# Performance work log

Measured on AMD Instinct MI355X. Metric: run time of the kernel, lower is better.

The kernel has to match this reference:

```python
import jax, jax.numpy as jnp
import numpy as np

EPS_LN = 1e-5
NEG_SLOPE = 0.2
NUM_GRAPHS = 64


def layer_norm(h, g, b):
    mu = h.mean(-1, keepdims=True)
    var = ((h - mu) ** 2).mean(-1, keepdims=True)
    return (h - mu) * jax.lax.rsqrt(var + EPS_LN) * g + b


def segment_softmax(alpha, dst, n):
    # alpha: [E2, H], softmax over edges sharing the same dst node
    m = jax.ops.segment_max(alpha, dst, num_segments=n)
    m = jnp.where(jnp.isfinite(m), m, 0.0)
    e = jnp.exp(alpha - m[dst])
    s = jax.ops.segment_sum(e, dst, num_segments=n)
    return e / (s[dst] + 1e-16)


def gat_conv(h, src, dst, eattr, W, We, a_s, a_d, a_e, bias, H, C):
    # PyG GATConv: shared src/dst linear, edge features, self-loops (fill='mean')
    N = h.shape[0]
    x = (h @ W).reshape(N, H, C)  # [N,H,C]
    loop = jnp.arange(N)
    src2 = jnp.concatenate([src, loop])
    dst2 = jnp.concatenate([dst, loop])
    loop_attr = jnp.broadcast_to(eattr.mean(0, keepdims=True), (N, eattr.shape[1]))
    e2 = jnp.concatenate([eattr, loop_attr], 0)
    eh = (e2 @ We).reshape(-1, H, C)  # [E2,H,C]
    alpha = (x * a_s).sum(-1)[src2] + (x * a_d).sum(-1)[dst2] + (eh * a_e).sum(-1)
    alpha = jax.nn.leaky_relu(alpha, NEG_SLOPE)  # [E2,H]
    alpha = segment_softmax(alpha, dst2, N)
    out = jax.ops.segment_sum(x[src2] * alpha[:, :, None], dst2, num_segments=N)
    return out.reshape(N, H * C) + bias


def setup_inputs():
    key = jax.random.key(0)
    ks = jax.random.split(key, 24)
    N, E = 50000, 400000
    Fin, Hd, H, ed = 6, 64, 4, 1
    d0 = Hd * H          # 256 after layer0
    C1 = 128 // H        # 32, layer1 per-head out
    s = 0.1
    inp = {
        'x': jax.random.normal(ks[0], (N, Fin), jnp.float32),
        'edge_index': jax.random.randint(ks[1], (2, E), 0, N),
        'edge_attr': jax.random.uniform(ks[2], (E, ed), jnp.float32),
        'batch': jnp.sort(jax.random.randint(ks[3], (N,), 0, NUM_GRAPHS)),
        'W_in': jax.random.normal(ks[4], (Fin, Hd), jnp.float32) * s,
        'b_in': jnp.zeros((Hd,), jnp.float32),
        'l0_W': jax.random.normal(ks[5], (Hd, H * Hd), jnp.float32) * s,
        'l0_We': jax.random.normal(ks[6], (ed, H * Hd), jnp.float32) * s,
        'l0_as': jax.random.normal(ks[7], (H, Hd), jnp.float32) * s,
        'l0_ad': jax.random.normal(ks[8], (H, Hd), jnp.float32) * s,
        'l0_ae': jax.random.normal(ks[9], (H, Hd), jnp.float32) * s,
        'l0_b': jnp.zeros((H * Hd,), jnp.float32),
        'ln0_g': jnp.ones((d0,), jnp.float32),
        'ln0_b': jnp.zeros((d0,), jnp.float32),
        'l1_W': jax.random.normal(ks[10], (d0, H * C1), jnp.float32) * s,
        'l1_We': jax.random.normal(ks[11], (ed, H * C1), jnp.float32) * s,
        'l1_as': jax.random.normal(ks[12], (H, C1), jnp.float32) * s,
        'l1_ad': jax.random.normal(ks[13], (H, C1), jnp.float32) * s,
        'l1_ae': jax.random.normal(ks[14], (H, C1), jnp.float32) * s,
        'l1_b': jnp.zeros((H * C1,), jnp.float32),
        'ln1_g': jnp.ones((128,), jnp.float32),
        'ln1_b': jnp.zeros((128,), jnp.float32),
    }
    return inp


def reference(x, edge_index, edge_attr, batch, W_in, b_in,
              l0_W, l0_We, l0_as, l0_ad, l0_ae, l0_b, ln0_g, ln0_b,
              l1_W, l1_We, l1_as, l1_ad, l1_ae, l1_b, ln1_g, ln1_b):
    src, dst = edge_index[0], edge_index[1]
    H = 4
    h = x @ W_in + b_in                                  # input_proj
    h = gat_conv(h, src, dst, edge_attr, l0_W, l0_We, l0_as, l0_ad, l0_ae, l0_b, H, 64)
    h = layer_norm(h, ln0_g, ln0_b)
    h = jax.nn.elu(h)                                    # dropout off (eval)
    h = gat_conv(h, src, dst, edge_attr, l1_W, l1_We, l1_as, l1_ad, l1_ae, l1_b, H, 32)
    h = layer_norm(h, ln1_g, ln1_b)
    cnt = jax.ops.segment_sum(jnp.ones((h.shape[0],), h.dtype), batch, num_segments=NUM_GRAPHS)
    h_mean = jax.ops.segment_sum(h, batch, num_segments=NUM_GRAPHS) / jnp.maximum(cnt, 1.0)[:, None]
    h_max = jax.ops.segment_max(h, batch, num_segments=NUM_GRAPHS)
    return (h_mean + h_max) / 2.0
```

## Files before the change

### kernel.cpp

```cpp
#include <hip/hip_runtime.h>
#include <math.h>

#define EPS_LN   1e-5f
#define NEG_SLOPE 0.2f
#define NUM_GRAPHS 64
#define POOL_SPLIT 16

__device__ __forceinline__ float red64(float v) {
    #pragma unroll
    for (int m = 32; m > 0; m >>= 1) v += __shfl_xor(v, m);
    return v;
}
__device__ __forceinline__ float red32(float v) {
    #pragma unroll
    for (int m = 16; m > 0; m >>= 1) v += __shfl_xor(v, m);
    return v;
}

__global__ __launch_bounds__(256) void k_input_proj(
    const float* __restrict__ x, const float* __restrict__ Win,
    const float* __restrict__ bin, float* __restrict__ h, int N)
{
    int t = blockIdx.x * 256 + threadIdx.x;
    if (t >= N * 64) return;
    int n = t >> 6, c = t & 63;
    float acc = bin[c];
    const float* xr = x + n * 6;
    #pragma unroll
    for (int k = 0; k < 6; ++k) acc += xr[k] * Win[k * 64 + c];
    h[t] = acc;
}

__global__ __launch_bounds__(256) void k_prep(
    const float* __restrict__ We0, const float* __restrict__ ae0,
    const float* __restrict__ We1, const float* __restrict__ ae1,
    float* __restrict__ wedot0, float* __restrict__ wedot1)
{
    __shared__ float red[256];
    int t = threadIdx.x;
    red[t] = We0[t] * ae0[t];
    __syncthreads();
    for (int s = 32; s > 0; s >>= 1) { if ((t & 63) < s) red[t] += red[t + s]; __syncthreads(); }
    if ((t & 63) == 0) wedot0[t >> 6] = red[t];
    __syncthreads();
    red[t] = (t < 128) ? We1[t] * ae1[t] : 0.f;
    __syncthreads();
    for (int s = 16; s > 0; s >>= 1) { if (t < 128 && (t & 31) < s) red[t] += red[t + s]; __syncthreads(); }
    if (t < 128 && (t & 31) == 0) wedot1[t >> 5] = red[t];
}

__global__ __launch_bounds__(256) void k_esum_partial(const float* __restrict__ ea, float* __restrict__ part, int E)
{
    __shared__ float red[256];
    int t = threadIdx.x;
    float s = 0.f;
    for (int i = blockIdx.x * 256 + t; i < E; i += gridDim.x * 256) s += ea[i];
    red[t] = s; __syncthreads();
    for (int k = 128; k > 0; k >>= 1) { if (t < k) red[t] += red[t + k]; __syncthreads(); }
    if (t == 0) part[blockIdx.x] = red[0];
}
__global__ __launch_bounds__(256) void k_esum_final(const float* __restrict__ part, int B, float* __restrict__ mean_out, int E)
{
    __shared__ float red[256];
    int t = threadIdx.x;
    red[t] = (t < B) ? part[t] : 0.f; __syncthreads();
    for (int k = 128; k > 0; k >>= 1) { if (t < k) red[t] += red[t + k]; __syncthreads(); }
    if (t == 0) *mean_out = red[0] / (float)E;
}

__global__ __launch_bounds__(256) void k_counts_init(int* __restrict__ counts, int N)
{
    int t = blockIdx.x * 256 + threadIdx.x;
    if (t < N) counts[t] = 1;
}
__global__ __launch_bounds__(256) void k_count(const int* __restrict__ dst, int* __restrict__ counts, int E)
{
    int e = blockIdx.x * 256 + threadIdx.x;
    if (e < E) atomicAdd(&counts[dst[e]], 1);
}
__global__ __launch_bounds__(256) void k_scan_partial(const int* __restrict__ counts, int* __restrict__ bsum, int N)
{
    __shared__ int red[256];
    int b = blockIdx.x, t = threadIdx.x;
    int base = b * 1024 + t * 4;
    int s = 0;
    #pragma unroll
    for (int i = 0; i < 4; ++i) { int idx = base + i; if (idx < N) s += counts[idx]; }
    red[t] = s; __syncthreads();
    for (int k = 128; k > 0; k >>= 1) { if (t < k) red[t] += red[t + k]; __syncthreads(); }
    if (t == 0) bsum[b] = red[0];
}
__global__ __launch_bounds__(64) void k_scan_bsums(const int* __restrict__ bsum, int* __restrict__ bpre, int B)
{
    __shared__ int s[64];
    int t = threadIdx.x;
    int v = (t < B) ? bsum[t] : 0;
    s[t] = v; __syncthreads();
    for (int off = 1; off < 64; off <<= 1) {
        int u = (t >= off) ? s[t - off] : 0; __syncthreads();
        s[t] += u; __syncthreads();
    }
    if (t < B) bpre[t] = s[t] - v;
}
__global__ __launch_bounds__(256) void k_scan_chunk(
    const int* __restrict__ counts, const int* __restrict__ bpre,
    int* __restrict__ row_ptr, int N, int E2)
{
    __shared__ int s[256];
    int b = blockIdx.x, t = threadIdx.x;
    int base = b * 1024 + t * 4;
    int l0 = (base + 0 < N) ? counts[base + 0] : 0;
    int l1 = (base + 1 < N) ? counts[base + 1] : 0;
    int l2 = (base + 2 < N) ? counts[base + 2] : 0;
    int l3 = (base + 3 < N) ? counts[base + 3] : 0;
    int lsum = l0 + l1 + l2 + l3;
    s[t] = lsum; __syncthreads();
    for (int off = 1; off < 256; off <<= 1) {
        int u = (t >= off) ? s[t - off] : 0; __syncthreads();
        s[t] += u; __syncthreads();
    }
    int run = bpre[b] + s[t] - lsum;
    if (base + 0 < N) row_ptr[base + 0] = run; run += l0;
    if (base + 1 < N) row_ptr[base + 1] = run; run += l1;
    if (base + 2 < N) row_ptr[base + 2] = run; run += l2;
    if (base + 3 < N) row_ptr[base + 3] = run;
    if (b == 0 && t == 0) row_ptr[N] = E2;
}
__global__ __launch_bounds__(256) void k_cursor_init(const int* __restrict__ row_ptr, int* __restrict__ cursor, int N)
{
    int t = blockIdx.x * 256 + threadIdx.x;
    if (t < N) cursor[t] = row_ptr[t];
}
__global__ __launch_bounds__(256) void k_place(
    const int* __restrict__ dst, int* __restrict__ cursor, int* __restrict__ eids, int E, int N)
{
    int e = blockIdx.x * 256 + threadIdx.x;
    if (e >= E + N) return;
    int d = (e < E) ? dst[e] : (e - E);
    int pos = atomicAdd(&cursor[d], 1);
    eids[pos] = e;
}
__global__ __launch_bounds__(256) void k_rowsort(const int* __restrict__ row_ptr, int* __restrict__ eids, int N)
{
    int n = blockIdx.x * 256 + threadIdx.x;
    if (n >= N) return;
    int r0 = row_ptr[n], r1 = row_ptr[n + 1];
    for (int i = r0 + 1; i < r1; ++i) {
        int key = eids[i];
        int j = i - 1;
        while (j >= r0 && eids[j] > key) { eids[j + 1] = eids[j]; --j; }
        eids[j + 1] = key;
    }
}

#define G0_NPW 4
__global__ __launch_bounds__(256) void k_gemm0(
    const float* __restrict__ h, const float* __restrict__ W0, float* __restrict__ x0, int N)
{
    __shared__ float Wl[64 * 256];
    int t = threadIdx.x;
    for (int i = t; i < 64 * 256; i += 256) Wl[i] = W0[i];
    __syncthreads();
    int wave = t >> 6, lane = t & 63;
    int gw = blockIdx.x * 4 + wave;
    int stride = gridDim.x * 4 * G0_NPW;
    for (int nb = gw * G0_NPW; nb < N; nb += stride) {
        float hv[G0_NPW];
        float acc[G0_NPW][4] = {};
        #pragma unroll
        for (int p = 0; p < G0_NPW; ++p) {
            int n = nb + p;
            hv[p] = (n < N) ? h[(size_t)n * 64 + lane] : 0.f;
        }
        for (int k = 0; k < 64; ++k) {
            float w0 = Wl[k * 256 + lane];
            float w1 = Wl[k * 256 + lane + 64];
            float w2 = Wl[k * 256 + lane + 128];
            float w3 = Wl[k * 256 + lane + 192];
            #pragma unroll
            for (int p = 0; p < G0_NPW; ++p) {
                float hk = __shfl(hv[p], k);
                acc[p][0] += hk * w0; acc[p][1] += hk * w1;
                acc[p][2] += hk * w2; acc[p][3] += hk * w3;
            }
        }
        #pragma unroll
        for (int p = 0; p < G0_NPW; ++p) {
            int n = nb + p;
            if (n < N) {
                float* o = x0 + (size_t)n * 256;
                o[lane] = acc[p][0]; o[lane + 64] = acc[p][1];
                o[lane + 128] = acc[p][2]; o[lane + 192] = acc[p][3];
            }
        }
    }
}

__global__ __launch_bounds__(256) void k_gemm1(
    const float* __restrict__ h0, const float* __restrict__ W1,
    float* __restrict__ x1, int N)
{
    __shared__ float Wc[32 * 128];
    __shared__ float Ht[32 * 128];
    const int nb = blockIdx.x * 128;
    const int t = threadIdx.x;
    const int tc = t & 15, tr = t >> 4;
    const int r0 = tr * 4, c0 = tc * 4;
    const int kg = t & 7, rb = t >> 3;
    float acc[8][8] = {};
    for (int kc = 0; kc < 8; ++kc) {
        __syncthreads();
        #pragma unroll
        for (int j = 0; j < 4; ++j) {
            int row = rb + j * 32;
            int n = nb + row;
            float4 v = make_float4(0.f, 0.f, 0.f, 0.f);
            if (n < N)
                v = *reinterpret_cast<const float4*>(h0 + (size_t)n * 256 + kc * 32 + kg * 4);
            #pragma unroll
            for (int i = 0; i < 4; ++i) {
                int k = kg * 4 + i;
                float e = (i == 0) ? v.x : (i == 1) ? v.y : (i == 2) ? v.z : v.w;
                Ht[k * 128 + (row ^ (k & 28))] = e;
            }
        }
        #pragma unroll
        for (int it = 0; it < 4; ++it) {
            int idx = t * 4 + it * 1024;
            int k2 = idx >> 7, c = idx & 127;
            *reinterpret_cast<float4*>(&Wc[idx]) =
                *reinterpret_cast<const float4*>(W1 + (size_t)(kc * 32 + k2) * 128 + c);
        }
        __syncthreads();
        #pragma unroll 4
        for (int k2 = 0; k2 < 32; ++k2) {
            int sw = k2 & 28;
            float4 hlo = *reinterpret_cast<const float4*>(&Ht[k2 * 128 + (r0 ^ sw)]);
            float4 hhi = *reinterpret_cast<const float4*>(&Ht[k2 * 128 + ((r0 + 64) ^ sw)]);
            float4 wlo = *reinterpret_cast<const float4*>(&Wc[k2 * 128 + c0]);
            float4 whi = *reinterpret_cast<const float4*>(&Wc[k2 * 128 + c0 + 64]);
            float hr[8] = {hlo.x, hlo.y, hlo.z, hlo.w, hhi.x, hhi.y, hhi.z, hhi.w};
            float wr[8] = {wlo.x, wlo.y, wlo.z, wlo.w, whi.x, whi.y, whi.z, whi.w};
            #pragma unroll
            for (int i = 0; i < 8; ++i)
                #pragma unroll
                for (int j = 0; j < 8; ++j)
                    acc[i][j] += hr[i] * wr[j];
        }
    }
    #pragma unroll
    for (int i = 0; i < 8; ++i) {
        int n = nb + ((i < 4) ? (r0 + i) : (r0 + 60 + i));
        if (n < N) {
            *reinterpret_cast<float4*>(x1 + (size_t)n * 128 + c0) =
                make_float4(acc[i][0], acc[i][1], acc[i][2], acc[i][3]);
            *reinterpret_cast<float4*>(x1 + (size_t)n * 128 + c0 + 64) =
                make_float4(acc[i][4], acc[i][5], acc[i][6], acc[i][7]);
        }
    }
}

template <int HC>
__global__ __launch_bounds__(256) void k_attn(
    const float* __restrict__ x, const float* __restrict__ a_s, const float* __restrict__ a_d,
    float* __restrict__ as_n, float* __restrict__ ad_n, int N)
{
    int n = (blockIdx.x * 256 + threadIdx.x) >> 6;
    int lane = threadIdx.x & 63;
    if (n >= N) return;
    const float* xr = x + (size_t)n * HC;
    #pragma unroll
    for (int j = 0; j < HC / 64; ++j) {
        int ch = j * 64 + lane;
        float v = xr[ch];
        float ps = v * a_s[ch], pd = v * a_d[ch];
        if (HC == 256) {
            ps = red64(ps); pd = red64(pd);
            if (lane == 0) { as_n[n * 4 + j] = ps; ad_n[n * 4 + j] = pd; }
        } else {
            ps = red32(ps); pd = red32(pd);
            if ((lane & 31) == 0) {
                int hh = 2 * j + (lane >> 5);
                as_n[n * 4 + hh] = ps; ad_n[n * 4 + hh] = pd;
            }
        }
    }
}

template <bool WRITE_SRC>
__global__ __launch_bounds__(256) void k_edgeprep(
    const int* __restrict__ row_ptr, const int* __restrict__ eids,
    const int* __restrict__ src, const float* __restrict__ eattr,
    const float* __restrict__ emean_p, const float* __restrict__ wedot,
    const float* __restrict__ as_n, const float* __restrict__ ad_n,
    int* __restrict__ srcp, float4* __restrict__ alpha, int N, int E)
{
    int n = (blockIdx.x * 256 + threadIdx.x) >> 6;
    int lane = threadIdx.x & 63;
    if (n >= N) return;
    float emean = *emean_p;
    float wd0 = wedot[0], wd1 = wedot[1], wd2 = wedot[2], wd3 = wedot[3];
    float adv0 = ad_n[n * 4 + 0], adv1 = ad_n[n * 4 + 1];
    float adv2 = ad_n[n * 4 + 2], adv3 = ad_n[n * 4 + 3];
    int r0 = row_ptr[n], r1 = row_ptr[n + 1];
    for (int i = r0 + lane; i < r1; i += 64) {
        int eid = eids[i];
        int sn; float ev;
        if (eid < E) { sn = src[eid]; ev = eattr[eid]; } else { sn = n; ev = emean; }
        if (WRITE_SRC) srcp[i] = sn;
        const float* as4 = as_n + (size_t)sn * 4;
        float a0 = as4[0] + adv0 + ev * wd0;
        float a1 = as4[1] + adv1 + ev * wd1;
        float a2 = as4[2] + adv2 + ev * wd2;
        float a3 = as4[3] + adv3 + ev * wd3;
        a0 = (a0 > 0.f) ? a0 : NEG_SLOPE * a0;
        a1 = (a1 > 0.f) ? a1 : NEG_SLOPE * a1;
        a2 = (a2 > 0.f) ? a2 : NEG_SLOPE * a2;
        a3 = (a3 > 0.f) ? a3 : NEG_SLOPE * a3;
        alpha[i] = make_float4(a0, a1, a2, a3);
    }
}

template <int HC, int VEC, bool DO_ELU>
__global__ __launch_bounds__(256) void k_agg(
    const float* __restrict__ x, const int* __restrict__ row_ptr,
    const int* __restrict__ srcp, const float* __restrict__ alpha,
    const float* __restrict__ bias, const float* __restrict__ lng, const float* __restrict__ lnb,
    float* __restrict__ out, int N)
{
    int n = (blockIdx.x * 256 + threadIdx.x) >> 6;
    int lane = threadIdx.x & 63;
    if (n >= N) return;
    int hh = lane >> 4;
    int r0 = row_ptr[n], r1 = row_ptr[n + 1];

    float m = -INFINITY, s = 0.f;
    float acc[VEC] = {};
    for (int i = r0; i < r1; ++i) {
        int sn = srcp[i];
        float a = alpha[(size_t)i * 4 + hh];
        float nm = fmaxf(m, a);
        float sc = __expf(m - nm);
        float w  = __expf(a - nm);
        m = nm;
        s = s * sc + w;
        const float* xr = x + (size_t)sn * HC + lane * VEC;
        if constexpr (VEC == 4) {
            float4 xv = *reinterpret_cast<const float4*>(xr);
            acc[0] = acc[0] * sc + w * xv.x;
            acc[1] = acc[1] * sc + w * xv.y;
            acc[2] = acc[2] * sc + w * xv.z;
            acc[3] = acc[3] * sc + w * xv.w;
        } else {
            float2 xv = *reinterpret_cast<const float2*>(xr);
            acc[0] = acc[0] * sc + w * xv.x;
            acc[1] = acc[1] * sc + w * xv.y;
        }
    }
    float inv = 1.f / (s + 1e-16f);

    int ch0 = lane * VEC;
    float v[VEC];
    #pragma unroll
    for (int i = 0; i < VEC; ++i) v[i] = acc[i] * inv + bias[ch0 + i];
    float ls = 0.f;
    #pragma unroll
    for (int i = 0; i < VEC; ++i) ls += v[i];
    ls = red64(ls);
    float mu = ls / (float)HC;
    float lv = 0.f;
    #pragma unroll
    for (int i = 0; i < VEC; ++i) { float d = v[i] - mu; lv += d * d; }
    lv = red64(lv);
    float rs = rsqrtf(lv / (float)HC + EPS_LN);
    float o[VEC];
    #pragma unroll
    for (int i = 0; i < VEC; ++i) {
        float y = (v[i] - mu) * rs * lng[ch0 + i] + lnb[ch0 + i];
        if (DO_ELU) y = (y > 0.f) ? y : (expm1f(y));
        o[i] = y;
    }
    float* orow = out + (size_t)n * HC + ch0;
    if constexpr (VEC == 4) *reinterpret_cast<float4*>(orow) = make_float4(o[0], o[1], o[2], o[3]);
    else                    *reinterpret_cast<float2*>(orow) = make_float2(o[0], o[1]);
}

__global__ __launch_bounds__(128) void k_bounds(const int* __restrict__ batch, int* __restrict__ gstart, int N)
{
    int g = threadIdx.x;
    if (g > NUM_GRAPHS) return;
    int lo = 0, hi = N;
    while (lo < hi) { int mid = (lo + hi) >> 1; if (batch[mid] < g) lo = mid + 1; else hi = mid; }
    gstart[g] = lo;
}
__global__ __launch_bounds__(128) void k_pool1(
    const float* __restrict__ h1, const int* __restrict__ gstart,
    float* __restrict__ psum, float* __restrict__ pmax)
{
    int g = blockIdx.x, sl = blockIdx.y, c = threadIdx.x;
    int s0 = gstart[g], s1 = gstart[g + 1];
    int cnt = s1 - s0;
    int chunk = (cnt + POOL_SPLIT - 1) / POOL_SPLIT;
    int b0 = s0 + sl * chunk;
    int b1 = min(b0 + chunk, s1);
    float sum = 0.f, mx = -INFINITY;
    for (int n = b0; n < b1; ++n) {
        float v = h1[(size_t)n * 128 + c];
        sum += v; mx = fmaxf(mx, v);
    }
    int o = (g * POOL_SPLIT + sl) * 128 + c;
    psum[o] = sum; pmax[o] = mx;
}
__global__ __launch_bounds__(128) void k_pool2(
    const float* __restrict__ psum, const float* __restrict__ pmax,
    const int* __restrict__ gstart, float* __restrict__ out)
{
    int g = blockIdx.x, c = threadIdx.x;
    float sum = 0.f, mx = -INFINITY;
    #pragma unroll
    for (int sl = 0; sl < POOL_SPLIT; ++sl) {
        int o = (g * POOL_SPLIT + sl) * 128 + c;
        sum += psum[o];
        mx = fmaxf(mx, pmax[o]);
    }
    int cnt = gstart[g + 1] - gstart[g];
    float mean = sum / fmaxf((float)cnt, 1.f);
    out[g * 128 + c] = 0.5f * (mean + mx);
}

extern "C" void kernel_launch(void* const* d_in, const int* in_sizes, int n_in,
                              void* d_out, int out_size, void* d_ws, size_t ws_size,
                              hipStream_t stream)
{
    const float* x     = (const float*)d_in[0];
    const int*   ei    = (const int*)d_in[1];
    const float* eattr = (const float*)d_in[2];
    const int*   batch = (const int*)d_in[3];
    const float* Win   = (const float*)d_in[4];
    const float* bin   = (const float*)d_in[5];
    const float* l0W   = (const float*)d_in[6];
    const float* l0We  = (const float*)d_in[7];
    const float* l0as  = (const float*)d_in[8];
    const float* l0ad  = (const float*)d_in[9];
    const float* l0ae  = (const float*)d_in[10];
    const float* l0b   = (const float*)d_in[11];
    const float* ln0g  = (const float*)d_in[12];
    const float* ln0b  = (const float*)d_in[13];
    const float* l1W   = (const float*)d_in[14];
    const float* l1We  = (const float*)d_in[15];
    const float* l1as  = (const float*)d_in[16];
    const float* l1ad  = (const float*)d_in[17];
    const float* l1ae  = (const float*)d_in[18];
    const float* l1b   = (const float*)d_in[19];
    const float* ln1g  = (const float*)d_in[20];
    const float* ln1b  = (const float*)d_in[21];

    const int N = in_sizes[0] / 6;
    const int E = in_sizes[1] / 2;
    const int E2 = E + N;
    const int* srcI = ei;
    const int* dstI = ei + E;

    char* ws = (char*)d_ws;
    size_t off = 0;
    auto alloc = [&](size_t bytes) -> char* {
        char* p = ws + off;
        off += (bytes + 255) & ~(size_t)255;
        return p;
    };

    float* h      = (float*)alloc((size_t)N * 64 * 4);
    float* x0     = (float*)alloc((size_t)N * 256 * 4);
    float* h0     = (float*)alloc((size_t)N * 256 * 4);
    float* as0    = (float*)alloc((size_t)N * 4 * 4);
    float* ad0    = (float*)alloc((size_t)N * 4 * 4);
    float* as1    = (float*)alloc((size_t)N * 4 * 4);
    float* ad1    = (float*)alloc((size_t)N * 4 * 4);
    int*   row_ptr= (int*)alloc((size_t)(N + 1) * 4);
    int*   counts = (int*)alloc((size_t)N * 4);
    int*   cursor = (int*)alloc((size_t)N * 4);
    int*   eids   = (int*)alloc((size_t)E2 * 4);
    int*   srcp   = (int*)alloc((size_t)E2 * 4);
    float4* alphab= (float4*)alloc((size_t)E2 * 16);
    int*   bsum   = (int*)alloc(64 * 4);
    int*   bpre   = (int*)alloc(64 * 4);
    float* epart  = (float*)alloc(256 * 4);
    float* emean  = (float*)alloc(4);
    float* wedot0 = (float*)alloc(16);
    float* wedot1 = (float*)alloc(16);
    int*   gstart = (int*)alloc((NUM_GRAPHS + 1) * 4);
    float* psum   = (float*)alloc((size_t)NUM_GRAPHS * POOL_SPLIT * 128 * 4);
    float* pmax   = (float*)alloc((size_t)NUM_GRAPHS * POOL_SPLIT * 128 * 4);

    float* x1 = x0;
    float* h1 = x0 + (size_t)N * 128;

    const int B = (N + 1023) / 1024;

    k_input_proj<<<(N * 64 + 255) / 256, 256, 0, stream>>>(x, Win, bin, h, N);
    k_prep<<<1, 256, 0, stream>>>(l0We, l0ae, l1We, l1ae, wedot0, wedot1);
    k_esum_partial<<<256, 256, 0, stream>>>(eattr, epart, E);
    k_esum_final<<<1, 256, 0, stream>>>(epart, 256, emean, E);

    k_counts_init<<<(N + 255) / 256, 256, 0, stream>>>(counts, N);
    k_count<<<(E + 255) / 256, 256, 0, stream>>>(dstI, counts, E);
    k_scan_partial<<<B, 256, 0, stream>>>(counts, bsum, N);
    k_scan_bsums<<<1, 64, 0, stream>>>(bsum, bpre, B);
    k_scan_chunk<<<B, 256, 0, stream>>>(counts, bpre, row_ptr, N, E2);
    k_cursor_init<<<(N + 255) / 256, 256, 0, stream>>>(row_ptr, cursor, N);
    k_place<<<(E2 + 255) / 256, 256, 0, stream>>>(dstI, cursor, eids, E, N);
    k_rowsort<<<(N + 255) / 256, 256, 0, stream>>>(row_ptr, eids, N);

    k_gemm0<<<512, 256, 0, stream>>>(h, l0W, x0, N);
    k_attn<256><<<(N + 3) / 4, 256, 0, stream>>>(x0, l0as, l0ad, as0, ad0, N);
    k_edgeprep<true><<<(N + 3) / 4, 256, 0, stream>>>(
        row_ptr, eids, srcI, eattr, emean, wedot0, as0, ad0, srcp, alphab, N, E);
    k_agg<256, 4, true><<<(N + 3) / 4, 256, 0, stream>>>(
        x0, row_ptr, srcp, (const float*)alphab, l0b, ln0g, ln0b, h0, N);

    k_gemm1<<<(N + 127) / 128, 256, 0, stream>>>(h0, l1W, x1, N);
    k_attn<128><<<(N + 3) / 4, 256, 0, stream>>>(x1, l1as, l1ad, as1, ad1, N);
    k_edgeprep<false><<<(N + 3) / 4, 256, 0, stream>>>(
        row_ptr, eids, srcI, eattr, emean, wedot1, as1, ad1, srcp, alphab, N, E);
    k_agg<128, 2, false><<<(N + 3) / 4, 256, 0, stream>>>(
        x1, row_ptr, srcp, (const float*)alphab, l1b, ln1g, ln1b, h1, N);

    k_bounds<<<1, 128, 0, stream>>>(batch, gstart, N);
    k_pool1<<<dim3(NUM_GRAPHS, POOL_SPLIT), 128, 0, stream>>>(h1, gstart, psum, pmax);
    k_pool2<<<NUM_GRAPHS, 128, 0, stream>>>(psum, pmax, gstart, (float*)d_out);
}
```

Measured before the change: 443.9 us.

## Precompute normalized softmax weights in edgeprep, simplify aggregation loop

The per-destination segment softmax moves out of the aggregation kernel and into the edge-prep kernel. There each wavefront does an online max/sum across its lanes, reduces it with shuffles, and rewrites alpha as normalized weights. The aggregation loop then does plain FMAs with no per-edge exp, rescale or serial max dependency. In exchange, edge-prep makes a second pass that reads and writes alpha, and the exp work runs once per edge-head rather than 64 times redundantly across lanes.

```diff
diff --git a/kernel.cpp b/kernel.cpp
--- a/kernel.cpp
+++ b/kernel.cpp
@@ -303,21 +303,51 @@
     float adv0 = ad_n[n * 4 + 0], adv1 = ad_n[n * 4 + 1];
     float adv2 = ad_n[n * 4 + 2], adv3 = ad_n[n * 4 + 3];
     int r0 = row_ptr[n], r1 = row_ptr[n + 1];
+
+    float m[4] = {-1e30f, -1e30f, -1e30f, -1e30f};
+    float s[4] = {0.f, 0.f, 0.f, 0.f};
     for (int i = r0 + lane; i < r1; i += 64) {
         int eid = eids[i];
         int sn; float ev;
         if (eid < E) { sn = src[eid]; ev = eattr[eid]; } else { sn = n; ev = emean; }
         if (WRITE_SRC) srcp[i] = sn;
         const float* as4 = as_n + (size_t)sn * 4;
-        float a0 = as4[0] + adv0 + ev * wd0;
-        float a1 = as4[1] + adv1 + ev * wd1;
-        float a2 = as4[2] + adv2 + ev * wd2;
-        float a3 = as4[3] + adv3 + ev * wd3;
-        a0 = (a0 > 0.f) ? a0 : NEG_SLOPE * a0;
-        a1 = (a1 > 0.f) ? a1 : NEG_SLOPE * a1;
-        a2 = (a2 > 0.f) ? a2 : NEG_SLOPE * a2;
-        a3 = (a3 > 0.f) ? a3 : NEG_SLOPE * a3;
-        alpha[i] = make_float4(a0, a1, a2, a3);
+        float a[4];
+        a[0] = as4[0] + adv0 + ev * wd0;
+        a[1] = as4[1] + adv1 + ev * wd1;
+        a[2] = as4[2] + adv2 + ev * wd2;
+        a[3] = as4[3] + adv3 + ev * wd3;
+        #pragma unroll
+        for (int hdx = 0; hdx < 4; ++hdx) {
+            float av = a[hdx];
+            av = (av > 0.f) ? av : NEG_SLOPE * av;
+            a[hdx] = av;
+            float nm = fmaxf(m[hdx], av);
+            s[hdx] = s[hdx] * __expf(m[hdx] - nm) + __expf(av - nm);
+            m[hdx] = nm;
+        }
+        alpha[i] = make_float4(a[0], a[1], a[2], a[3]);
+    }
+    #pragma unroll
+    for (int off = 32; off > 0; off >>= 1) {
+        #pragma unroll
+        for (int hdx = 0; hdx < 4; ++hdx) {
+            float om = __shfl_xor(m[hdx], off);
+            float os = __shfl_xor(s[hdx], off);
+            float nm = fmaxf(m[hdx], om);
+            s[hdx] = s[hdx] * __expf(m[hdx] - nm) + os * __expf(om - nm);
+            m[hdx] = nm;
+        }
+    }
+    float inv[4];
+    #pragma unroll
+    for (int hdx = 0; hdx < 4; ++hdx) inv[hdx] = 1.f / (s[hdx] + 1e-16f);
+    for (int i = r0 + lane; i < r1; i += 64) {
+        float4 a = alpha[i];
+        alpha[i] = make_float4(__expf(a.x - m[0]) * inv[0],
+                               __expf(a.y - m[1]) * inv[1],
+                               __expf(a.z - m[2]) * inv[2],
+                               __expf(a.w - m[3]) * inv[3]);
     }
 }
 
@@ -334,35 +364,25 @@
     int hh = lane >> 4;
     int r0 = row_ptr[n], r1 = row_ptr[n + 1];
 
-    float m = -INFINITY, s = 0.f;
     float acc[VEC] = {};
     for (int i = r0; i < r1; ++i) {
         int sn = srcp[i];
-        float a = alpha[(size_t)i * 4 + hh];
-        float nm = fmaxf(m, a);
-        float sc = __expf(m - nm);
-        float w  = __expf(a - nm);
-        m = nm;
-        s = s * sc + w;
+        float w = alpha[(size_t)i * 4 + hh];
         const float* xr = x + (size_t)sn * HC + lane * VEC;
         if constexpr (VEC == 4) {
             float4 xv = *reinterpret_cast<const float4*>(xr);
-            acc[0] = acc[0] * sc + w * xv.x;
-            acc[1] = acc[1] * sc + w * xv.y;
-            acc[2] = acc[2] * sc + w * xv.z;
-            acc[3] = acc[3] * sc + w * xv.w;
+            acc[0] += w * xv.x; acc[1] += w * xv.y;
+            acc[2] += w * xv.z; acc[3] += w * xv.w;
         } else {
             float2 xv = *reinterpret_cast<const float2*>(xr);
-            acc[0] = acc[0] * sc + w * xv.x;
-            acc[1] = acc[1] * sc + w * xv.y;
-        }
-    }
-    float inv = 1.f / (s + 1e-16f);
+            acc[0] += w * xv.x; acc[1] += w * xv.y;
+        }
+    }
 
     int ch0 = lane * VEC;
     float v[VEC];
     #pragma unroll
-    for (int i = 0; i < VEC; ++i) v[i] = acc[i] * inv + bias[ch0 + i];
+    for (int i = 0; i < VEC; ++i) v[i] = acc[i] + bias[ch0 + i];
     float ls = 0.f;
     #pragma unroll
     for (int i = 0; i < VEC; ++i) ls += v[i];
```

Result: slower. 480.6 us (+8.3%).

## Precompute segment softmax weights in edgeprep and batch gathers in aggregation

Applied to the files above, without the earlier changes.

Edge-prep now computes the per-destination max and exponentials across the warp, stores unnormalised weights plus a per-node reciprocal sum, and aggregation becomes a plain weighted sum. Aggregation also loads 8 source indices and weights up front so the row gathers can be in flight together. This drops the serial online-softmax rescaling and the per-edge exponentials from the memory-bound aggregation loop. The cost is a second pass over alpha in edge-prep and an extra small buffer.

```diff
diff --git a/kernel.cpp b/kernel.cpp
--- a/kernel.cpp
+++ b/kernel.cpp
@@ -293,7 +293,8 @@
     const int* __restrict__ src, const float* __restrict__ eattr,
     const float* __restrict__ emean_p, const float* __restrict__ wedot,
     const float* __restrict__ as_n, const float* __restrict__ ad_n,
-    int* __restrict__ srcp, float4* __restrict__ alpha, int N, int E)
+    int* __restrict__ srcp, float4* __restrict__ alpha, float* __restrict__ sinv,
+    int N, int E)
 {
     int n = (blockIdx.x * 256 + threadIdx.x) >> 6;
     int lane = threadIdx.x & 63;
@@ -303,6 +304,8 @@
     float adv0 = ad_n[n * 4 + 0], adv1 = ad_n[n * 4 + 1];
     float adv2 = ad_n[n * 4 + 2], adv3 = ad_n[n * 4 + 3];
     int r0 = row_ptr[n], r1 = row_ptr[n + 1];
+
+    float m0 = -1e30f, m1 = -1e30f, m2 = -1e30f, m3 = -1e30f;
     for (int i = r0 + lane; i < r1; i += 64) {
         int eid = eids[i];
         int sn; float ev;
@@ -317,7 +320,35 @@
         a1 = (a1 > 0.f) ? a1 : NEG_SLOPE * a1;
         a2 = (a2 > 0.f) ? a2 : NEG_SLOPE * a2;
         a3 = (a3 > 0.f) ? a3 : NEG_SLOPE * a3;
+        m0 = fmaxf(m0, a0); m1 = fmaxf(m1, a1);
+        m2 = fmaxf(m2, a2); m3 = fmaxf(m3, a3);
         alpha[i] = make_float4(a0, a1, a2, a3);
+    }
+    #pragma unroll
+    for (int off = 32; off > 0; off >>= 1) {
+        m0 = fmaxf(m0, __shfl_xor(m0, off));
+        m1 = fmaxf(m1, __shfl_xor(m1, off));
+        m2 = fmaxf(m2, __shfl_xor(m2, off));
+        m3 = fmaxf(m3, __shfl_xor(m3, off));
+    }
+    float s0 = 0.f, s1 = 0.f, s2 = 0.f, s3 = 0.f;
+    for (int i = r0 + lane; i < r1; i += 64) {
+        float4 a = alpha[i];
+        float w0 = __expf(a.x - m0), w1 = __expf(a.y - m1);
+        float w2 = __expf(a.z - m2), w3 = __expf(a.w - m3);
+        s0 += w0; s1 += w1; s2 += w2; s3 += w3;
+        alpha[i] = make_float4(w0, w1, w2, w3);
+    }
+    #pragma unroll
+    for (int off = 32; off > 0; off >>= 1) {
+        s0 += __shfl_xor(s0, off); s1 += __shfl_xor(s1, off);
+        s2 += __shfl_xor(s2, off); s3 += __shfl_xor(s3, off);
+    }
+    if (lane == 0) {
+        sinv[n * 4 + 0] = 1.f / (s0 + 1e-16f);
+        sinv[n * 4 + 1] = 1.f / (s1 + 1e-16f);
+        sinv[n * 4 + 2] = 1.f / (s2 + 1e-16f);
+        sinv[n * 4 + 3] = 1.f / (s3 + 1e-16f);
     }
 }
 
@@ -325,6 +356,7 @@
 __global__ __launch_bounds__(256) void k_agg(
     const float* __restrict__ x, const int* __restrict__ row_ptr,
     const int* __restrict__ srcp, const float* __restrict__ alpha,
+    const float* __restrict__ sinv,
     const float* __restrict__ bias, const float* __restrict__ lng, const float* __restrict__ lnb,
     float* __restrict__ out, int N)
 {
@@ -334,30 +366,28 @@
     int hh = lane >> 4;
     int r0 = row_ptr[n], r1 = row_ptr[n + 1];
 
-    float m = -INFINITY, s = 0.f;
     float acc[VEC] = {};
-    for (int i = r0; i < r1; ++i) {
-        int sn = srcp[i];
-        float a = alpha[(size_t)i * 4 + hh];
-        float nm = fmaxf(m, a);
-        float sc = __expf(m - nm);
-        float w  = __expf(a - nm);
-        m = nm;
-        s = s * sc + w;
-        const float* xr = x + (size_t)sn * HC + lane * VEC;
-        if constexpr (VEC == 4) {
-            float4 xv = *reinterpret_cast<const float4*>(xr);
-            acc[0] = acc[0] * sc + w * xv.x;
-            acc[1] = acc[1] * sc + w * xv.y;
-            acc[2] = acc[2] * sc + w * xv.z;
-            acc[3] = acc[3] * sc + w * xv.w;
-        } else {
-            float2 xv = *reinterpret_cast<const float2*>(xr);
-            acc[0] = acc[0] * sc + w * xv.x;
-            acc[1] = acc[1] * sc + w * xv.y;
-        }
-    }
-    float inv = 1.f / (s + 1e-16f);
+    for (int i = r0; i < r1; i += 8) {
+        int cnt = min(r1 - i, 8);
+        int sn[8]; float wv[8];
+        #pragma unroll
+        for (int j = 0; j < 8; ++j)
+            if (j < cnt) { sn[j] = srcp[i + j]; wv[j] = alpha[(size_t)(i + j) * 4 + hh]; }
+        #pragma unroll
+        for (int j = 0; j < 8; ++j)
+            if (j < cnt) {
+                const float* xr = x + (size_t)sn[j] * HC + lane * VEC;
+                if constexpr (VEC == 4) {
+                    float4 xv = *reinterpret_cast<const float4*>(xr);
+                    acc[0] += wv[j] * xv.x; acc[1] += wv[j] * xv.y;
+                    acc[2] += wv[j] * xv.z; acc[3] += wv[j] * xv.w;
+                } else {
+                    float2 xv = *reinterpret_cast<const float2*>(xr);
+                    acc[0] += wv[j] * xv.x; acc[1] += wv[j] * xv.y;
+                }
+            }
+    }
+    float inv = sinv[n * 4 + hh];
 
     int ch0 = lane * VEC;
     float v[VEC];
@@ -476,6 +506,7 @@
     float* ad0    = (float*)alloc((size_t)N * 4 * 4);
     float* as1    = (float*)alloc((size_t)N * 4 * 4);
     float* ad1    = (float*)alloc((size_t)N * 4 * 4);
+    float* sinv   = (float*)alloc((size_t)N * 4 * 4);
     int*   row_ptr= (int*)alloc((size_t)(N + 1) * 4);
     int*   counts = (int*)alloc((size_t)N * 4);
     int*   cursor = (int*)alloc((size_t)N * 4);
@@ -514,16 +545,16 @@
     k_gemm0<<<512, 256, 0, stream>>>(h, l0W, x0, N);
     k_attn<256><<<(N + 3) / 4, 256, 0, stream>>>(x0, l0as, l0ad, as0, ad0, N);
     k_edgeprep<true><<<(N + 3) / 4, 256, 0, stream>>>(
-        row_ptr, eids, srcI, eattr, emean, wedot0, as0, ad0, srcp, alphab, N, E);
+        row_ptr, eids, srcI, eattr, emean, wedot0, as0, ad0, srcp, alphab, sinv, N, E);
     k_agg<256, 4, true><<<(N + 3) / 4, 256, 0, stream>>>(
-        x0, row_ptr, srcp, (const float*)alphab, l0b, ln0g, ln0b, h0, N);
+        x0, row_ptr, srcp, (const float*)alphab, sinv, l0b, ln0g, ln0b, h0, N);
 
     k_gemm1<<<(N + 127) / 128, 256, 0, stream>>>(h0, l1W, x1, N);
     k_attn<128><<<(N + 3) / 4, 256, 0, stream>>>(x1, l1as, l1ad, as1, ad1, N);
     k_edgeprep<false><<<(N + 3) / 4, 256, 0, stream>>>(
-        row_ptr, eids, srcI, eattr, emean, wedot1, as1, ad1, srcp, alphab, N, E);
+        row_ptr, eids, srcI, eattr, emean, wedot1, as1, ad1, srcp, alphab, sinv, N, E);
     k_agg<128, 2, false><<<(N + 3) / 4, 256, 0, stream>>>(
-        x1, row_ptr, srcp, (const float*)alphab, l1b, ln1g, ln1b, h1, N);
+        x1, row_ptr, srcp, (const float*)alphab, sinv, l1b, ln1g, ln1b, h1, N);
 
     k_bounds<<<1, 128, 0, stream>>>(batch, gstart, N);
     k_pool1<<<dim3(NUM_GRAPHS, POOL_SPLIT), 128, 0, stream>>>(h1, gstart, psum, pmax);
```

New measurement: 457.4 us. +3.0%, slower.
